# Performance work log

Measured on AMD Instinct MI355X. Metric: run time of the kernel, lower is better.

## Reference

```python
import jax, jax.numpy as jnp
import numpy as np
import math

E = 1024
H = 16
D = E // H  # head_dim = 64


def setup_inputs() -> dict:
    key = jax.random.key(0)
    ks = jax.random.split(key, 12)
    B, N = 2, 2048
    x = jax.random.normal(ks[0], (B, N, E), dtype=jnp.float32)
    region_mask = jax.random.randint(ks[1], (B, N), 0, 2).astype(jnp.float32)
    attn_mask = jax.random.randint(ks[2], (B, N, N), 0, 2).astype(bool)
    std = 0.02
    Wq = jax.random.normal(ks[3], (E, E), dtype=jnp.float32) * std
    Wk = jax.random.normal(ks[4], (E, E), dtype=jnp.float32) * std
    Wv = jax.random.normal(ks[5], (E, E), dtype=jnp.float32) * std
    Wo = jax.random.normal(ks[6], (E, E), dtype=jnp.float32) * std
    bq = jnp.zeros((E,), jnp.float32)
    bk = jnp.zeros((E,), jnp.float32)
    bv = jnp.zeros((E,), jnp.float32)
    bo = jnp.zeros((E,), jnp.float32)
    region_bias = jax.random.normal(ks[7], (1, H, 1, 1), dtype=jnp.float32) * std
    return {"x": x, "region_mask": region_mask, "attn_mask": attn_mask,
            "Wq": Wq, "bq": bq, "Wk": Wk, "bk": bk, "Wv": Wv, "bv": bv,
            "Wo": Wo, "bo": bo, "region_bias": region_bias}


def reference(x, region_mask, attn_mask, Wq, bq, Wk, bk, Wv, bv, Wo, bo, region_bias):
    B, N, _ = x.shape
    # projections (torch Linear: y = x @ W.T + b), split heads -> (B, H, N, D)
    def split_heads(y):
        return y.reshape(B, N, H, D).transpose(0, 2, 1, 3)
    q = split_heads(x @ Wq.T + bq)
    k = split_heads(x @ Wk.T + bk)
    v = split_heads(x @ Wv.T + bv)
    # eager scores (B, H, N, N)
    scores = jnp.einsum('bhqd,bhkd->bhqk', q, k) / math.sqrt(D)
    # additive regional bias: (1,H,1,1) * (B,1,N,1) broadcasts over keys
    scores = scores + region_bias * region_mask[:, None, :, None]
    # masked_fill(attn_mask, -inf); mask is (B,N,N) -> (B,1,N,N)
    scores = jnp.where(attn_mask[:, None, :, :], -jnp.inf, scores)
    w = jax.nn.softmax(scores, axis=-1)  # dropout is identity in eval
    out = jnp.einsum('bhqk,bhkd->bhqd', w, v)
    out = out.transpose(0, 2, 1, 3).reshape(B, N, E)
    return out @ Wo.T + bo
```

## Files before the change

kernel.cpp:

```cpp
#include <hip/hip_runtime.h>
#include <hip/hip_bf16.h>
#include <stdint.h>

typedef __hip_bfloat16 bf16;
typedef unsigned long long u64;
typedef __attribute__((ext_vector_type(4))) float f32x4;
typedef __attribute__((ext_vector_type(8))) short short8;

#define MFMA16 __builtin_amdgcn_mfma_f32_16x16x32_bf16

constexpr int Bc = 2, Nc = 2048, Ec = 1024, Hc = 16, Dc = 64;
constexpr int Mc = Bc * Nc;
constexpr int Kc = Ec;

constexpr size_t OFF_XB   = 256;
constexpr size_t SZ_XE    = (size_t)Mc * Ec * 2;
constexpr size_t SZ_W     = (size_t)Ec * Ec * 2;
constexpr size_t OFF_WQB  = OFF_XB  + SZ_XE;
constexpr size_t OFF_WKB  = OFF_WQB + SZ_W;
constexpr size_t OFF_WVB  = OFF_WKB + SZ_W;
constexpr size_t OFF_WOB  = OFF_WVB + SZ_W;
constexpr size_t OFF_QB   = OFF_WOB + SZ_W;
constexpr size_t OFF_KB   = OFF_QB  + SZ_XE;
constexpr size_t OFF_VTB  = OFF_KB  + SZ_XE;
constexpr size_t OFF_OB   = OFF_VTB + SZ_XE;
constexpr size_t OFF_MP   = OFF_OB  + SZ_XE;

#define QSCALE 0.18033688f

__device__ __forceinline__ void gld16(const void* g, void* l) {
  __builtin_amdgcn_global_load_lds((const __attribute__((address_space(1))) void*)g,
                                   (__attribute__((address_space(3))) void*)l,
                                   16, 0, 0);
}

__device__ __forceinline__ float fexp2(float x) {
#if __has_builtin(__builtin_amdgcn_exp2f)
  return __builtin_amdgcn_exp2f(x);
#else
  float r; asm("v_exp_f32 %0, %1" : "=v"(r) : "v"(x)); return r;
#endif
}

__device__ __forceinline__ unsigned cvt2(float a, float b) {
  __hip_bfloat162 h = __float22bfloat162_rn(float2{a, b});
  return *reinterpret_cast<unsigned*>(&h);
}

__device__ __forceinline__ unsigned nib4(unsigned x) {
  const unsigned b = ((x & 0x7F7F7F7Fu) + 0x7F7F7F7Fu) | x;
  return ((b >> 7) & 1u) | ((b >> 14) & 2u) | ((b >> 21) & 4u) | ((b >> 28) & 8u);
}

__global__ __launch_bounds__(256)
void prep(const unsigned char* __restrict__ mbytes,
          const float* __restrict__ x,  const float* __restrict__ wq,
          const float* __restrict__ wk, const float* __restrict__ wv,
          const float* __restrict__ wo,
          u64* __restrict__ packed,
          uint2* __restrict__ xb,  uint2* __restrict__ wqb,
          uint2* __restrict__ wkb, uint2* __restrict__ wvb,
          uint2* __restrict__ wob)
{
  if (blockIdx.x < 512) {
    __shared__ int found;
    if (threadIdx.x == 0) found = 0;
    __syncthreads();
    int loc = 0;
    for (int i = threadIdx.x; i < 4096; i += 256)
      if ((i & 3) && mbytes[i] == 1) loc = 1;
    if (loc) atomicOr(&found, 1);
    __syncthreads();
    const bool bytem = (found != 0);

    const int widx = blockIdx.x * 256 + threadIdx.x;
    u64 bits = 0;
    if (bytem) {
      const uint4* src = (const uint4*)(mbytes + (size_t)widx * 64);
#pragma unroll
      for (int i = 0; i < 4; ++i) {
        const uint4 v = src[i];
        bits |= (u64)nib4(v.x) << (16 * i + 0);
        bits |= (u64)nib4(v.y) << (16 * i + 4);
        bits |= (u64)nib4(v.z) << (16 * i + 8);
        bits |= (u64)nib4(v.w) << (16 * i + 12);
      }
    } else {
      const uint4* src = (const uint4*)mbytes + (size_t)widx * 16;
#pragma unroll
      for (int i = 0; i < 16; ++i) {
        const uint4 v = src[i];
        const unsigned n = (v.x != 0 ? 1u : 0u) | (v.y != 0 ? 2u : 0u) |
                           (v.z != 0 ? 4u : 0u) | (v.w != 0 ? 8u : 0u);
        bits |= (u64)n << (4 * i);
      }
    }
    packed[widx] = bits;
    return;
  }
  const long XG = (long)Mc * Ec / 4;
  const long WG = (long)Ec * Ec / 4;
  const long total = XG + 4 * WG;
  const long nthr = (long)(gridDim.x - 512) * 256;
  for (long g = (long)(blockIdx.x - 512) * 256 + threadIdx.x; g < total; g += nthr) {
    const float* src; uint2* dst; long r;
    if (g < XG)              { src = x;  dst = xb;  r = g; }
    else if (g < XG + WG)    { src = wq; dst = wqb; r = g - XG; }
    else if (g < XG + 2*WG)  { src = wk; dst = wkb; r = g - XG - WG; }
    else if (g < XG + 3*WG)  { src = wv; dst = wvb; r = g - XG - 2*WG; }
    else                     { src = wo; dst = wob; r = g - XG - 3*WG; }
    float4 v = reinterpret_cast<const float4*>(src)[r];
    uint2 o;
    o.x = cvt2(v.x, v.y);
    o.y = cvt2(v.z, v.w);
    dst[r] = o;
  }
}

template<int BN>
__device__ __forceinline__ void gemm_core(const bf16* __restrict__ A,
                                          const bf16* __restrict__ Bw,
                                          int bm, int bn,
                                          bf16* As0, bf16* As1,
                                          bf16* Bs0, bf16* Bs1,
                                          f32x4 (&acc)[4][BN / 32])
{
  constexpr int NJ = BN / 32;
  const int t = threadIdx.x, lane = t & 63, w = t >> 6;
  const int wr = w >> 1, wc = w & 1;
  const int llo = lane & 15, lhi = lane >> 4;
  const int srow = t >> 3, schunk = t & 7;
  const int sswz = schunk ^ (srow & 7);
  const bf16* aSrc = A  + (size_t)(bm * 128 + srow) * Kc + sswz * 8;
  const bf16* bSrc = Bw + (size_t)(bn * BN  + srow) * Kc + sswz * 8;

  auto stage = [&](bf16* Asb, bf16* Bsb, int kt) {
    char* ldsA = (char*)Asb + w * 1024;
    char* ldsB = (char*)Bsb + w * 1024;
#pragma unroll
    for (int i = 0; i < 4; ++i)
      gld16(aSrc + (size_t)i * 32 * Kc + kt, ldsA + i * 4096);
#pragma unroll
    for (int i = 0; i < BN / 32; ++i)
      gld16(bSrc + (size_t)i * 32 * Kc + kt, ldsB + i * 4096);
  };

  stage(As0, Bs0, 0);
  __syncthreads();

  for (int kti = 0; kti < Kc / 64; ++kti) {
    const bool even = !(kti & 1);
    const char* Asc = (const char*)(even ? As0 : As1);
    const char* Bsc = (const char*)(even ? Bs0 : Bs1);
    if (kti + 1 < Kc / 64)
      stage(even ? As1 : As0, even ? Bs1 : Bs0, (kti + 1) * 64);
#pragma unroll
    for (int kk = 0; kk < 2; ++kk) {
      short8 af[4], bg[NJ];
      const int chunk = (kk * 4 + lhi) ^ (lane & 7);
#pragma unroll
      for (int i = 0; i < 4; ++i) {
        const int rowa = wr * 64 + i * 16 + llo;
        af[i] = *(const short8*)(Asc + rowa * 128 + chunk * 16);
      }
#pragma unroll
      for (int j = 0; j < NJ; ++j) {
        const int rowb = wc * (BN / 2) + j * 16 + llo;
        bg[j] = *(const short8*)(Bsc + rowb * 128 + chunk * 16);
      }
#pragma unroll
      for (int i = 0; i < 4; ++i)
#pragma unroll
        for (int j = 0; j < NJ; ++j)
          acc[i][j] = MFMA16(af[i], bg[j], acc[i][j], 0, 0, 0);
    }
    __syncthreads();
  }
}

__global__ __launch_bounds__(256)
void gemm_qkv(const bf16* __restrict__ xb,
              const bf16* __restrict__ wq, const bf16* __restrict__ wk,
              const bf16* __restrict__ wv,
              const float* __restrict__ bq, const float* __restrict__ bk,
              const float* __restrict__ bv,
              bf16* __restrict__ Q, bf16* __restrict__ Ko, bf16* __restrict__ VT)
{
  __shared__ bf16 As[2][128 * 64], Bs[2][64 * 64];
  const int sel = blockIdx.x >> 9, inner = blockIdx.x & 511;
  const int bm = inner >> 4, bn = inner & 15;
  const bf16*  W    = sel == 0 ? wq : (sel == 1 ? wk : wv);
  const float* bias = sel == 0 ? bq : (sel == 1 ? bk : bv);
  f32x4 acc[4][2] = {};
  gemm_core<64>(xb, W, bm, bn, As[0], As[1], Bs[0], Bs[1], acc);

  const int t = threadIdx.x, lane = t & 63, w = t >> 6;
  const int wr = w >> 1, wc = w & 1;
  const int llo = lane & 15, lhi = lane >> 4;
#pragma unroll
  for (int i = 0; i < 4; ++i)
#pragma unroll
    for (int j = 0; j < 2; ++j)
#pragma unroll
      for (int r = 0; r < 4; ++r) {
        const int m = bm * 128 + wr * 64 + i * 16 + lhi * 4 + r;
        const int e = bn * 64 + wc * 32 + j * 16 + llo;
        float v = acc[i][j][r] + bias[e];
        if (sel == 0) {
          Q[(size_t)m * Ec + e] = __float2bfloat16(v * QSCALE);
        } else if (sel == 1) {
          Ko[(size_t)m * Ec + e] = __float2bfloat16(v);
        } else {
          const int b = m >> 11, n = m & 2047, h = e >> 6, d = e & 63;
          VT[(((size_t)(b * Hc + h)) * Dc + d) * Nc + n] = __float2bfloat16(v);
        }
      }
}

__global__ __launch_bounds__(256)
void gemm_out(const bf16* __restrict__ ob, const bf16* __restrict__ wo,
              const float* __restrict__ bo, float* __restrict__ out)
{
  __shared__ bf16 As[2][128 * 64], Bs[2][64 * 64];
  const int bm = blockIdx.x >> 4, bn = blockIdx.x & 15;
  f32x4 acc[4][2] = {};
  gemm_core<64>(ob, wo, bm, bn, As[0], As[1], Bs[0], Bs[1], acc);

  const int t = threadIdx.x, lane = t & 63, w = t >> 6;
  const int wr = w >> 1, wc = w & 1;
  const int llo = lane & 15, lhi = lane >> 4;
#pragma unroll
  for (int i = 0; i < 4; ++i)
#pragma unroll
    for (int j = 0; j < 2; ++j)
#pragma unroll
      for (int r = 0; r < 4; ++r) {
        const int m = bm * 128 + wr * 64 + i * 16 + lhi * 4 + r;
        const int e = bn * 64 + wc * 32 + j * 16 + llo;
        out[(size_t)m * Ec + e] = acc[i][j][r] + bo[e];
      }
}

__global__ __launch_bounds__(256, 3)
void flash_attn(const bf16* __restrict__ Q, const bf16* __restrict__ Kb,
                const bf16* __restrict__ VT, const u64* __restrict__ mpack,
                bf16* __restrict__ O)
{
  __shared__ bf16 Ks[2][64 * 64];
  __shared__ bf16 Vs[2][64 * 64];
  __shared__ bf16 Ps[4][32 * 64];
  const int t = threadIdx.x, lane = t & 63, w = t >> 6;
  const int bh = blockIdx.x >> 4, qt = blockIdx.x & 15;
  const int b = bh >> 4, h = bh & 15;
  const int q0 = qt * 128 + w * 32;
  const int llo = lane & 15, lhi = lane >> 4;
  const int swz = (lane & 7) << 4;

  short8 aq00, aq01, aq10, aq11;
  {
    const bf16* qb0 = Q + ((size_t)(b * Nc + q0 + llo)) * Ec + h * Dc + lhi * 8;
    aq00 = *(const short8*)qb0;
    aq01 = *(const short8*)(qb0 + 32);
    const bf16* qb1 = qb0 + (size_t)16 * Ec;
    aq10 = *(const short8*)qb1;
    aq11 = *(const short8*)(qb1 + 32);
  }

  const short8 kOnes = {16256,16256,16256,16256,16256,16256,16256,16256};
  const f32x4 fz = {};
  f32x4 oacc0[4] = {}, oacc1[4] = {};
  f32x4 lacc0 = {}, lacc1 = {};

  const int srow = t >> 3, schunk = t & 7;
  const int sswz = schunk ^ (srow & 7);
  const bf16* kSrc = Kb + ((size_t)(b * Nc + srow)) * Ec + h * Dc + sswz * 8;
  const bf16* vSrc = VT + ((size_t)(bh * Dc + srow)) * Nc + sswz * 8;

  const u64* mrow0 = mpack + ((size_t)(b * Nc) + q0 + llo) * (Nc / 64);
  const u64* mrow1 = mrow0 + (size_t)16 * (Nc / 64);

  auto stage = [&](int buf, int kt) {
    gld16(kSrc + (size_t)kt * Ec,        (char*)Ks[buf] + w * 1024);
    gld16(kSrc + (size_t)(kt + 32) * Ec, (char*)Ks[buf] + 4096 + w * 1024);
    gld16(vSrc + kt,                     (char*)Vs[buf] + w * 1024);
    gld16(vSrc + (size_t)32 * Nc + kt,   (char*)Vs[buf] + 4096 + w * 1024);
  };

  char* prow0 = (char*)Ps[w] + llo * 128;
  char* prow1 = prow0 + 16 * 128;

  auto body = [&](const char* KsC, const char* VsC, u64 mw0, u64 mw1) {
    f32x4 s0[4], s1[4];
    __builtin_amdgcn_s_setprio(1);
#pragma unroll
    for (int f = 0; f < 4; ++f) {
      const int row = f * 16 + llo;
      short8 kb0 = *(const short8*)(KsC + row * 128 + ((lhi * 16) ^ swz));
      short8 kb1 = *(const short8*)(KsC + row * 128 + (((4 + lhi) * 16) ^ swz));
      s0[f] = MFMA16(kb0, aq00, fz, 0, 0, 0);
      s0[f] = MFMA16(kb1, aq01, s0[f], 0, 0, 0);
      s1[f] = MFMA16(kb0, aq10, fz, 0, 0, 0);
      s1[f] = MFMA16(kb1, aq11, s1[f], 0, 0, 0);
    }
    __builtin_amdgcn_s_setprio(0);

    {
      const unsigned mlo = (unsigned)(mw0 >> (lhi * 4));
      const unsigned mhi = (unsigned)(mw0 >> (lhi * 4 + 32));
#pragma unroll
      for (int f = 0; f < 4; ++f) {
        const unsigned mf = (f < 2 ? (mlo >> (f * 16)) : (mhi >> ((f - 2) * 16)));
#pragma unroll
        for (int r = 0; r < 4; ++r) {
          const float p = fexp2(s0[f][r]);
          s0[f][r] = ((mf >> r) & 1u) ? 0.f : p;
        }
      }
    }
    {
      const unsigned mlo = (unsigned)(mw1 >> (lhi * 4));
      const unsigned mhi = (unsigned)(mw1 >> (lhi * 4 + 32));
#pragma unroll
      for (int f = 0; f < 4; ++f) {
        const unsigned mf = (f < 2 ? (mlo >> (f * 16)) : (mhi >> ((f - 2) * 16)));
#pragma unroll
        for (int r = 0; r < 4; ++r) {
          const float p = fexp2(s1[f][r]);
          s1[f][r] = ((mf >> r) & 1u) ? 0.f : p;
        }
      }
    }

#pragma unroll
    for (int f = 0; f < 4; ++f) {
      uint2 pk0, pk1;
      pk0.x = cvt2(s0[f][0], s0[f][1]); pk0.y = cvt2(s0[f][2], s0[f][3]);
      pk1.x = cvt2(s1[f][0], s1[f][1]); pk1.y = cvt2(s1[f][2], s1[f][3]);
      *(uint2*)(prow0 + ((f * 32 + lhi * 8) ^ swz)) = pk0;
      *(uint2*)(prow1 + ((f * 32 + lhi * 8) ^ swz)) = pk1;
    }
    asm volatile("s_waitcnt lgkmcnt(0)" ::: "memory");

    short8 pa00 = *(const short8*)(prow0 + ((lhi * 16) ^ swz));
    short8 pa01 = *(const short8*)(prow0 + ((64 + lhi * 16) ^ swz));
    short8 pa10 = *(const short8*)(prow1 + ((lhi * 16) ^ swz));
    short8 pa11 = *(const short8*)(prow1 + ((64 + lhi * 16) ^ swz));

    __builtin_amdgcn_s_setprio(1);
#pragma unroll
    for (int df = 0; df < 4; ++df) {
      const int row = df * 16 + llo;
      short8 vb0 = *(const short8*)(VsC + row * 128 + ((lhi * 16) ^ swz));
      short8 vb1 = *(const short8*)(VsC + row * 128 + (((4 + lhi) * 16) ^ swz));
      oacc0[df] = MFMA16(pa00, vb0, oacc0[df], 0, 0, 0);
      oacc0[df] = MFMA16(pa01, vb1, oacc0[df], 0, 0, 0);
      oacc1[df] = MFMA16(pa10, vb0, oacc1[df], 0, 0, 0);
      oacc1[df] = MFMA16(pa11, vb1, oacc1[df], 0, 0, 0);
    }
    lacc0 = MFMA16(pa00, kOnes, lacc0, 0, 0, 0);
    lacc0 = MFMA16(pa01, kOnes, lacc0, 0, 0, 0);
    lacc1 = MFMA16(pa10, kOnes, lacc1, 0, 0, 0);
    lacc1 = MFMA16(pa11, kOnes, lacc1, 0, 0, 0);
    __builtin_amdgcn_s_setprio(0);
  };

  stage(0, 0);
  __syncthreads();
  u64 mwA0 = mrow0[0], mwA1 = mrow1[0];

  for (int ti = 0; ti < Nc / 64; ti += 2) {
    if (ti + 1 < Nc / 64) stage(1, (ti + 1) * 64);
    const u64 mwB0 = (ti + 1 < Nc / 64) ? mrow0[ti + 1] : 0;
    const u64 mwB1 = (ti + 1 < Nc / 64) ? mrow1[ti + 1] : 0;
    body((const char*)Ks[0], (const char*)Vs[0], mwA0, mwA1);
    __syncthreads();
    if (ti + 2 < Nc / 64) stage(0, (ti + 2) * 64);
    const u64 mwN0 = (ti + 2 < Nc / 64) ? mrow0[ti + 2] : 0;
    const u64 mwN1 = (ti + 2 < Nc / 64) ? mrow1[ti + 2] : 0;
    body((const char*)Ks[1], (const char*)Vs[1], mwB0, mwB1);
    __syncthreads();
    mwA0 = mwN0; mwA1 = mwN1;
  }

  float inv0[4], inv1[4];
#pragma unroll
  for (int r = 0; r < 4; ++r) { inv0[r] = 1.0f / lacc0[r]; inv1[r] = 1.0f / lacc1[r]; }
#pragma unroll
  for (int df = 0; df < 4; ++df)
#pragma unroll
    for (int r = 0; r < 4; ++r) {
      const int e = h * Dc + df * 16 + llo;
      const int qa = q0 + lhi * 4 + r;
      O[((size_t)(b * Nc + qa)) * Ec + e] = __float2bfloat16(oacc0[df][r] * inv0[r]);
      O[((size_t)(b * Nc + qa + 16)) * Ec + e] = __float2bfloat16(oacc1[df][r] * inv1[r]);
    }
}

extern "C" void kernel_launch(void* const* d_in, const int* in_sizes, int n_in,
                              void* d_out, int out_size, void* d_ws, size_t ws_size,
                              hipStream_t stream)
{
  (void)in_sizes; (void)n_in; (void)out_size; (void)ws_size;
  const float* x  = (const float*)d_in[0];
  const void* mask = d_in[2];
  const float* Wq = (const float*)d_in[3];
  const float* bq = (const float*)d_in[4];
  const float* Wk = (const float*)d_in[5];
  const float* bk = (const float*)d_in[6];
  const float* Wv = (const float*)d_in[7];
  const float* bv = (const float*)d_in[8];
  const float* Wo = (const float*)d_in[9];
  const float* bo = (const float*)d_in[10];
  float* out = (float*)d_out;
  char* ws = (char*)d_ws;

  bf16* XB  = (bf16*)(ws + OFF_XB);
  bf16* WQB = (bf16*)(ws + OFF_WQB);
  bf16* WKB = (bf16*)(ws + OFF_WKB);
  bf16* WVB = (bf16*)(ws + OFF_WVB);
  bf16* WOB = (bf16*)(ws + OFF_WOB);
  bf16* QB  = (bf16*)(ws + OFF_QB);
  bf16* KB  = (bf16*)(ws + OFF_KB);
  bf16* VTB = (bf16*)(ws + OFF_VTB);
  bf16* OB  = (bf16*)(ws + OFF_OB);
  u64*  MP  = (u64*)(ws + OFF_MP);

  prep<<<512 + 1280, 256, 0, stream>>>((const unsigned char*)mask,
                                       x, Wq, Wk, Wv, Wo, MP,
                                       (uint2*)XB, (uint2*)WQB, (uint2*)WKB,
                                       (uint2*)WVB, (uint2*)WOB);
  gemm_qkv<<<1536, 256, 0, stream>>>(XB, WQB, WKB, WVB, bq, bk, bv, QB, KB, VTB);
  flash_attn<<<512, 256, 0, stream>>>(QB, KB, VTB, MP, OB);
  gemm_out<<<512, 256, 0, stream>>>(OB, WOB, bo, out);
}
```

Measured before the change: 143.5 us.

## Fuse QKV GEMM into one shared-A pass and split attention keys with combine

The QKV projection now computes Q, K and V tiles in one block that loads the X tile once and reuses it against three weight tiles, cutting redundant A loads and the block count. Flash attention moves to 512-thread blocks covering 256 queries, and when the workspace is large enough it splits the key range in two. Each half writes unnormalized fp32 partial outputs and row sums, and a new combine kernel merges and normalizes them. This adds an extra kernel launch, fp32 partial-buffer traffic and more register pressure in the fused GEMM, in exchange for more parallelism and better operand reuse.

```diff
diff --git a/kernel.cpp b/kernel.cpp
--- a/kernel.cpp
+++ b/kernel.cpp
@@ -25,6 +25,11 @@
 constexpr size_t OFF_VTB  = OFF_KB  + SZ_XE;
 constexpr size_t OFF_OB   = OFF_VTB + SZ_XE;
 constexpr size_t OFF_MP   = OFF_OB  + SZ_XE;
+constexpr size_t OFF_PART = OFF_MP + (size_t)(Bc * Nc) * (Nc / 64) * 8;
+constexpr size_t SZ_PART  = (size_t)2 * 32 * Nc * Dc * 4;
+constexpr size_t OFF_LS   = OFF_PART + SZ_PART;
+constexpr size_t SZ_LS    = (size_t)2 * 32 * Nc * 4;
+constexpr size_t WS_NEED  = OFF_LS + SZ_LS;
 
 #define QSCALE 0.18033688f
 
@@ -117,6 +122,99 @@
   }
 }
 
+__global__ __launch_bounds__(256)
+void gemm_qkv(const bf16* __restrict__ xb,
+              const bf16* __restrict__ wq, const bf16* __restrict__ wk,
+              const bf16* __restrict__ wv,
+              const float* __restrict__ bq, const float* __restrict__ bk,
+              const float* __restrict__ bv,
+              bf16* __restrict__ Q, bf16* __restrict__ Ko, bf16* __restrict__ VT)
+{
+  __shared__ bf16 As[2][128 * 64];
+  __shared__ bf16 Bs[2][3][64 * 64];
+  const int bm = blockIdx.x >> 4, bn = blockIdx.x & 15;
+  const int t = threadIdx.x, lane = t & 63, w = t >> 6;
+  const int wr = w >> 1, wc = w & 1;
+  const int llo = lane & 15, lhi = lane >> 4;
+  const int srow = t >> 3, schunk = t & 7;
+  const int sswz = schunk ^ (srow & 7);
+  const bf16* aSrc  = xb + (size_t)(bm * 128 + srow) * Kc + sswz * 8;
+  const bf16* bSrc0 = wq + (size_t)(bn * 64 + srow) * Kc + sswz * 8;
+  const bf16* bSrc1 = wk + (size_t)(bn * 64 + srow) * Kc + sswz * 8;
+  const bf16* bSrc2 = wv + (size_t)(bn * 64 + srow) * Kc + sswz * 8;
+
+  f32x4 acc[3][4][2] = {};
+
+  auto stage = [&](int buf, int kt) {
+    char* ldsA = (char*)As[buf] + w * 1024;
+#pragma unroll
+    for (int i = 0; i < 4; ++i)
+      gld16(aSrc + (size_t)i * 32 * Kc + kt, ldsA + i * 4096);
+#pragma unroll
+    for (int s = 0; s < 3; ++s) {
+      const bf16* bs = s == 0 ? bSrc0 : (s == 1 ? bSrc1 : bSrc2);
+      char* ldsB = (char*)Bs[buf][s] + w * 1024;
+      gld16(bs + kt, ldsB);
+      gld16(bs + (size_t)32 * Kc + kt, ldsB + 4096);
+    }
+  };
+
+  stage(0, 0);
+  __syncthreads();
+
+  for (int kti = 0; kti < Kc / 64; ++kti) {
+    const int cur = kti & 1;
+    if (kti + 1 < Kc / 64) stage(cur ^ 1, (kti + 1) * 64);
+    const char* Asc = (const char*)As[cur];
+#pragma unroll
+    for (int kk = 0; kk < 2; ++kk) {
+      const int chunk = (kk * 4 + lhi) ^ (lane & 7);
+      short8 af[4];
+#pragma unroll
+      for (int i = 0; i < 4; ++i) {
+        const int rowa = wr * 64 + i * 16 + llo;
+        af[i] = *(const short8*)(Asc + rowa * 128 + chunk * 16);
+      }
+#pragma unroll
+      for (int s = 0; s < 3; ++s) {
+        const char* Bsc = (const char*)Bs[cur][s];
+        const int rowb0 = wc * 32 + llo;
+        short8 bg0 = *(const short8*)(Bsc + rowb0 * 128 + chunk * 16);
+        short8 bg1 = *(const short8*)(Bsc + (rowb0 + 16) * 128 + chunk * 16);
+#pragma unroll
+        for (int i = 0; i < 4; ++i) {
+          acc[s][i][0] = MFMA16(af[i], bg0, acc[s][i][0], 0, 0, 0);
+          acc[s][i][1] = MFMA16(af[i], bg1, acc[s][i][1], 0, 0, 0);
+        }
+      }
+    }
+    __syncthreads();
+  }
+
+#pragma unroll
+  for (int s = 0; s < 3; ++s) {
+    const float* bias = s == 0 ? bq : (s == 1 ? bk : bv);
+#pragma unroll
+    for (int i = 0; i < 4; ++i)
+#pragma unroll
+      for (int j = 0; j < 2; ++j)
+#pragma unroll
+        for (int r = 0; r < 4; ++r) {
+          const int m = bm * 128 + wr * 64 + i * 16 + lhi * 4 + r;
+          const int e = bn * 64 + wc * 32 + j * 16 + llo;
+          float v = acc[s][i][j][r] + bias[e];
+          if (s == 0) {
+            Q[(size_t)m * Ec + e] = __float2bfloat16(v * QSCALE);
+          } else if (s == 1) {
+            Ko[(size_t)m * Ec + e] = __float2bfloat16(v);
+          } else {
+            const int b = m >> 11, n = m & 2047, h = e >> 6, d = e & 63;
+            VT[(((size_t)(b * Hc + h)) * Dc + d) * Nc + n] = __float2bfloat16(v);
+          }
+        }
+  }
+}
+
 template<int BN>
 __device__ __forceinline__ void gemm_core(const bf16* __restrict__ A,
                                           const bf16* __restrict__ Bw,
@@ -179,45 +277,6 @@
 }
 
 __global__ __launch_bounds__(256)
-void gemm_qkv(const bf16* __restrict__ xb,
-              const bf16* __restrict__ wq, const bf16* __restrict__ wk,
-              const bf16* __restrict__ wv,
-              const float* __restrict__ bq, const float* __restrict__ bk,
-              const float* __restrict__ bv,
-              bf16* __restrict__ Q, bf16* __restrict__ Ko, bf16* __restrict__ VT)
-{
-  __shared__ bf16 As[2][128 * 64], Bs[2][64 * 64];
-  const int sel = blockIdx.x >> 9, inner = blockIdx.x & 511;
-  const int bm = inner >> 4, bn = inner & 15;
-  const bf16*  W    = sel == 0 ? wq : (sel == 1 ? wk : wv);
-  const float* bias = sel == 0 ? bq : (sel == 1 ? bk : bv);
-  f32x4 acc[4][2] = {};
-  gemm_core<64>(xb, W, bm, bn, As[0], As[1], Bs[0], Bs[1], acc);
-
-  const int t = threadIdx.x, lane = t & 63, w = t >> 6;
-  const int wr = w >> 1, wc = w & 1;
-  const int llo = lane & 15, lhi = lane >> 4;
-#pragma unroll
-  for (int i = 0; i < 4; ++i)
-#pragma unroll
-    for (int j = 0; j < 2; ++j)
-#pragma unroll
-      for (int r = 0; r < 4; ++r) {
-        const int m = bm * 128 + wr * 64 + i * 16 + lhi * 4 + r;
-        const int e = bn * 64 + wc * 32 + j * 16 + llo;
-        float v = acc[i][j][r] + bias[e];
-        if (sel == 0) {
-          Q[(size_t)m * Ec + e] = __float2bfloat16(v * QSCALE);
-        } else if (sel == 1) {
-          Ko[(size_t)m * Ec + e] = __float2bfloat16(v);
-        } else {
-          const int b = m >> 11, n = m & 2047, h = e >> 6, d = e & 63;
-          VT[(((size_t)(b * Hc + h)) * Dc + d) * Nc + n] = __float2bfloat16(v);
-        }
-      }
-}
-
-__global__ __launch_bounds__(256)
 void gemm_out(const bf16* __restrict__ ob, const bf16* __restrict__ wo,
               const float* __restrict__ bo, float* __restrict__ out)
 {
@@ -241,20 +300,27 @@
       }
 }
 
-__global__ __launch_bounds__(256, 3)
+template<int NSPLIT>
+__global__ __launch_bounds__(512, 4)
 void flash_attn(const bf16* __restrict__ Q, const bf16* __restrict__ Kb,
                 const bf16* __restrict__ VT, const u64* __restrict__ mpack,
-                bf16* __restrict__ O)
+                bf16* __restrict__ O, float* __restrict__ part,
+                float* __restrict__ lsum)
 {
   __shared__ bf16 Ks[2][64 * 64];
   __shared__ bf16 Vs[2][64 * 64];
-  __shared__ bf16 Ps[4][32 * 64];
+  __shared__ bf16 Ps[8][32 * 64];
+  constexpr int NT = (Nc / 64) / NSPLIT;
   const int t = threadIdx.x, lane = t & 63, w = t >> 6;
-  const int bh = blockIdx.x >> 4, qt = blockIdx.x & 15;
+  const int inner = blockIdx.x & 255;
+  const int half = (NSPLIT == 2) ? (blockIdx.x >> 8) : 0;
+  const int bh = inner >> 3, qt = inner & 7;
   const int b = bh >> 4, h = bh & 15;
-  const int q0 = qt * 128 + w * 32;
+  const int q0 = qt * 256 + w * 32;
   const int llo = lane & 15, lhi = lane >> 4;
   const int swz = (lane & 7) << 4;
+  const int kt0 = half * (Nc / NSPLIT);
+  const int kw0 = kt0 >> 6;
 
   short8 aq00, aq01, aq10, aq11;
   {
@@ -280,10 +346,8 @@
   const u64* mrow1 = mrow0 + (size_t)16 * (Nc / 64);
 
   auto stage = [&](int buf, int kt) {
-    gld16(kSrc + (size_t)kt * Ec,        (char*)Ks[buf] + w * 1024);
-    gld16(kSrc + (size_t)(kt + 32) * Ec, (char*)Ks[buf] + 4096 + w * 1024);
-    gld16(vSrc + kt,                     (char*)Vs[buf] + w * 1024);
-    gld16(vSrc + (size_t)32 * Nc + kt,   (char*)Vs[buf] + 4096 + w * 1024);
+    gld16(kSrc + (size_t)kt * Ec, (char*)Ks[buf] + w * 1024);
+    gld16(vSrc + kt,              (char*)Vs[buf] + w * 1024);
   };
 
   char* prow0 = (char*)Ps[w] + llo * 128;
@@ -364,43 +428,81 @@
     __builtin_amdgcn_s_setprio(0);
   };
 
-  stage(0, 0);
+  stage(0, kt0);
   __syncthreads();
-  u64 mwA0 = mrow0[0], mwA1 = mrow1[0];
-
-  for (int ti = 0; ti < Nc / 64; ti += 2) {
-    if (ti + 1 < Nc / 64) stage(1, (ti + 1) * 64);
-    const u64 mwB0 = (ti + 1 < Nc / 64) ? mrow0[ti + 1] : 0;
-    const u64 mwB1 = (ti + 1 < Nc / 64) ? mrow1[ti + 1] : 0;
+  u64 mwA0 = mrow0[kw0], mwA1 = mrow1[kw0];
+
+  for (int ti = 0; ti < NT; ti += 2) {
+    if (ti + 1 < NT) stage(1, kt0 + (ti + 1) * 64);
+    const u64 mwB0 = (ti + 1 < NT) ? mrow0[kw0 + ti + 1] : 0;
+    const u64 mwB1 = (ti + 1 < NT) ? mrow1[kw0 + ti + 1] : 0;
     body((const char*)Ks[0], (const char*)Vs[0], mwA0, mwA1);
     __syncthreads();
-    if (ti + 2 < Nc / 64) stage(0, (ti + 2) * 64);
-    const u64 mwN0 = (ti + 2 < Nc / 64) ? mrow0[ti + 2] : 0;
-    const u64 mwN1 = (ti + 2 < Nc / 64) ? mrow1[ti + 2] : 0;
+    if (ti + 2 < NT) stage(0, kt0 + (ti + 2) * 64);
+    const u64 mwN0 = (ti + 2 < NT) ? mrow0[kw0 + ti + 2] : 0;
+    const u64 mwN1 = (ti + 2 < NT) ? mrow1[kw0 + ti + 2] : 0;
     body((const char*)Ks[1], (const char*)Vs[1], mwB0, mwB1);
     __syncthreads();
     mwA0 = mwN0; mwA1 = mwN1;
   }
 
-  float inv0[4], inv1[4];
-#pragma unroll
-  for (int r = 0; r < 4; ++r) { inv0[r] = 1.0f / lacc0[r]; inv1[r] = 1.0f / lacc1[r]; }
-#pragma unroll
-  for (int df = 0; df < 4; ++df)
-#pragma unroll
-    for (int r = 0; r < 4; ++r) {
-      const int e = h * Dc + df * 16 + llo;
-      const int qa = q0 + lhi * 4 + r;
-      O[((size_t)(b * Nc + qa)) * Ec + e] = __float2bfloat16(oacc0[df][r] * inv0[r]);
-      O[((size_t)(b * Nc + qa + 16)) * Ec + e] = __float2bfloat16(oacc1[df][r] * inv1[r]);
-    }
+  if constexpr (NSPLIT == 1) {
+    float inv0[4], inv1[4];
+#pragma unroll
+    for (int r = 0; r < 4; ++r) { inv0[r] = 1.0f / lacc0[r]; inv1[r] = 1.0f / lacc1[r]; }
+#pragma unroll
+    for (int df = 0; df < 4; ++df)
+#pragma unroll
+      for (int r = 0; r < 4; ++r) {
+        const int e = h * Dc + df * 16 + llo;
+        const int qa = q0 + lhi * 4 + r;
+        O[((size_t)(b * Nc + qa)) * Ec + e] = __float2bfloat16(oacc0[df][r] * inv0[r]);
+        O[((size_t)(b * Nc + qa + 16)) * Ec + e] = __float2bfloat16(oacc1[df][r] * inv1[r]);
+      }
+  } else {
+    const size_t rowbase = ((size_t)half * 32 + bh) * Nc;
+#pragma unroll
+    for (int df = 0; df < 4; ++df)
+#pragma unroll
+      for (int r = 0; r < 4; ++r) {
+        const int qa = q0 + lhi * 4 + r;
+        part[(rowbase + qa) * Dc + df * 16 + llo] = oacc0[df][r];
+        part[(rowbase + qa + 16) * Dc + df * 16 + llo] = oacc1[df][r];
+      }
+    if (llo == 0) {
+#pragma unroll
+      for (int r = 0; r < 4; ++r) {
+        lsum[rowbase + q0 + lhi * 4 + r] = lacc0[r];
+        lsum[rowbase + q0 + lhi * 4 + r + 16] = lacc1[r];
+      }
+    }
+  }
+}
+
+__global__ __launch_bounds__(256)
+void combine(const float* __restrict__ part, const float* __restrict__ lsum,
+             bf16* __restrict__ O)
+{
+  const int gid = blockIdx.x * 256 + threadIdx.x;
+  const int row = gid >> 4;
+  const int dq = gid & 15;
+  constexpr int ROWS = 32 * Nc;
+  const float4 p0 = *(const float4*)(part + (size_t)row * Dc + dq * 4);
+  const float4 p1 = *(const float4*)(part + ((size_t)ROWS + row) * Dc + dq * 4);
+  const float inv = 1.0f / (lsum[row] + lsum[ROWS + row]);
+  const int bh = row >> 11, n = row & 2047;
+  const int b = bh >> 4, h = bh & 15;
+  uint2 o;
+  o.x = cvt2((p0.x + p1.x) * inv, (p0.y + p1.y) * inv);
+  o.y = cvt2((p0.z + p1.z) * inv, (p0.w + p1.w) * inv);
+  *(uint2*)(O + ((size_t)(b * Nc + n)) * Ec + h * Dc + dq * 4) = o;
 }
 
 extern "C" void kernel_launch(void* const* d_in, const int* in_sizes, int n_in,
                               void* d_out, int out_size, void* d_ws, size_t ws_size,
                               hipStream_t stream)
 {
-  (void)in_sizes; (void)n_in; (void)out_size; (void)ws_size;
+  (void)in_sizes; (void)n_in; (void)out_size;
   const float* x  = (const float*)d_in[0];
   const void* mask = d_in[2];
   const float* Wq = (const float*)d_in[3];
@@ -424,12 +526,19 @@
   bf16* VTB = (bf16*)(ws + OFF_VTB);
   bf16* OB  = (bf16*)(ws + OFF_OB);
   u64*  MP  = (u64*)(ws + OFF_MP);
+  float* PART = (float*)(ws + OFF_PART);
+  float* LS   = (float*)(ws + OFF_LS);
 
   prep<<<512 + 1280, 256, 0, stream>>>((const unsigned char*)mask,
                                        x, Wq, Wk, Wv, Wo, MP,
                                        (uint2*)XB, (uint2*)WQB, (uint2*)WKB,
                                        (uint2*)WVB, (uint2*)WOB);
-  gemm_qkv<<<1536, 256, 0, stream>>>(XB, WQB, WKB, WVB, bq, bk, bv, QB, KB, VTB);
-  flash_attn<<<512, 256, 0, stream>>>(QB, KB, VTB, MP, OB);
+  gemm_qkv<<<512, 256, 0, stream>>>(XB, WQB, WKB, WVB, bq, bk, bv, QB, KB, VTB);
+  if (ws_size >= WS_NEED) {
+    flash_attn<2><<<512, 512, 0, stream>>>(QB, KB, VTB, MP, OB, PART, LS);
+    combine<<<4096, 256, 0, stream>>>(PART, LS, OB);
+  } else {
+    flash_attn<1><<<256, 512, 0, stream>>>(QB, KB, VTB, MP, OB, PART, LS);
+  }
   gemm_out<<<512, 256, 0, stream>>>(OB, WOB, bo, out);
 }
```

Result: no change. 142.7 us (-0.6%).
